# Performance work log

Hardware: AMD Instinct MI355X
Metric: run time of the kernel (lower is better)

## Reference

```python
import jax, jax.numpy as jnp
import numpy as np

D_MODEL = 768
BATCH = 4096
RANK_DIST = [(4, 512), (8, 256), (16, 128), (32, 64), (64, 32)]


@jax.custom_vjp
def jumprelu(x):
    # hard threshold at 0 in fwd; full straight-through estimator in bwd
    return x * (x > 0.0).astype(x.dtype)


def _jr_fwd(x):
    return jumprelu(x), None


def _jr_bwd(res, g):
    return (g,)


jumprelu.defvjp(_jr_fwd, _jr_bwd)


def setup_inputs() -> dict:
    key = jax.random.key(0)
    keys = jax.random.split(key, 1 + 3 * len(RANK_DIST))
    inp = {"x": jax.random.normal(keys[0], (BATCH, D_MODEL), dtype=jnp.float32)}
    for i, (n, r) in enumerate(RANK_DIST):
        kV, kU, kE = keys[1 + 3 * i], keys[2 + 3 * i], keys[3 + 3 * i]
        scale = (1.0 / (D_MODEL * r)) ** 0.25
        inp[f"V{i}"] = scale * jax.random.normal(kV, (n, r, D_MODEL), dtype=jnp.float32)
        inp[f"U{i}"] = scale * jax.random.normal(kU, (n, D_MODEL, r), dtype=jnp.float32)
        enc = jax.random.normal(kE, (n, D_MODEL), dtype=jnp.float32)
        inp[f"enc{i}"] = enc / jnp.linalg.norm(enc, axis=1, keepdims=True)
        inp[f"b{i}"] = jnp.full((n,), -1.0, dtype=jnp.float32)
    return inp


def _group_forward(x, V, U, enc, b):
    n, r, d = V.shape
    pre = x @ enc.T - b                      # (b, n)
    gate = jumprelu(pre)                     # (b, n)
    Vx = jnp.einsum("nrd,bd->nbr", V, x)    # (n, b, r)
    # fused: UVx gated by gate then summed over transforms n
    out = jnp.einsum("ndr,nbr,bn->bd", U, Vx, gate)  # (b, d)
    u_norms = jnp.linalg.norm(U.reshape(n, -1), axis=1)
    v_norms = jnp.linalg.norm(V.reshape(n, -1), axis=1)
    frob = u_norms * v_norms / jnp.sqrt(jnp.asarray(d * r, dtype=x.dtype))
    return out, gate, frob


def reference(x, V0, U0, enc0, b0, V1, U1, enc1, b1, V2, U2, enc2, b2,
              V3, U3, enc3, b3, V4, U4, enc4, b4):
    Vs = [V0, V1, V2, V3, V4]
    Us = [U0, U1, U2, U3, U4]
    encs = [enc0, enc1, enc2, enc3, enc4]
    bs = [b0, b1, b2, b3, b4]
    output = jnp.zeros_like(x)
    total_sparsity = jnp.asarray(0.0, dtype=x.dtype)
    total_active = jnp.asarray(0.0, dtype=x.dtype)
    gate_acts = []
    for V, U, enc, b in zip(Vs, Us, encs, bs):
        g_out, gate, frob = _group_forward(x, V, U, enc, b)
        output = output + g_out
        mean_abs_gate = jnp.abs(gate).mean(axis=0)
        total_sparsity = total_sparsity + (jnp.tanh(mean_abs_gate) * frob).sum()
        total_active = total_active + (gate > 0).astype(x.dtype).sum(axis=1).mean()
        gate_acts.append(gate)
    return (output, total_sparsity, total_active, *gate_acts)
```

## Files before the change

### kernel.cpp

```cpp
#include <hip/hip_runtime.h>

#define BATCH 4096
#define DM 768
#define LTOT 10240
#define NG 124

typedef __bf16 bf16x8 __attribute__((ext_vector_type(8)));
typedef short short8 __attribute__((ext_vector_type(8)));
typedef float f32x4 __attribute__((ext_vector_type(4)));
typedef float f32x16 __attribute__((ext_vector_type(16)));

struct Ptr5 { const float* p[5]; };

__device__ __forceinline__ unsigned short f2bf(float f) {
    unsigned u = __builtin_bit_cast(unsigned, f);
    unsigned r = (u + 0x7FFFu + ((u >> 16) & 1u)) >> 16;
    return (unsigned short)r;
}

__device__ __forceinline__ short8 pack8(float4 a, float4 b) {
    union { unsigned short u[8]; short8 s; } o;
    o.u[0] = f2bf(a.x); o.u[1] = f2bf(a.y); o.u[2] = f2bf(a.z); o.u[3] = f2bf(a.w);
    o.u[4] = f2bf(b.x); o.u[5] = f2bf(b.y); o.u[6] = f2bf(b.z); o.u[7] = f2bf(b.w);
    return o.s;
}


__global__ __launch_bounds__(256) void prep_k(const float* __restrict__ x,
                                              Ptr5 vp, Ptr5 up, Ptr5 ep, Ptr5 bp,
                                              unsigned short* __restrict__ vb,
                                              unsigned short* __restrict__ w2t,
                                              unsigned short* __restrict__ xb,
                                              float* __restrict__ gate_ws,
                                              float* __restrict__ outg,
                                              float* __restrict__ vslot,
                                              float* __restrict__ uslot,
                                              float* __restrict__ gslot,
                                              float* __restrict__ aslot) {
    const int basen[5] = {0, 4, 12, 28, 60};
    int bx = blockIdx.x;
    int tid = threadIdx.x;
    if (bx < 32) {
        __shared__ unsigned short lA[128 * 64];
        __shared__ unsigned short lB[128 * 64];
        __shared__ float sgs[128];
        __shared__ float sac;
        int wave = tid >> 6, lane = tid & 63;
        int wm = wave >> 1, wn = wave & 1;
        int lan15 = lane & 15, quad = lane >> 4;
        int sw = lan15 & 7;
        int m0 = bx * 128;
        f32x4 acc[4][4] = {};
        for (int k0 = 0; k0 < DM; k0 += 64) {
            __syncthreads();
            #pragma unroll
            for (int i = 0; i < 4; i++) {
                int gidx = i * 256 + tid;
                int row = gidx >> 3, kb = gidx & 7;
                int r7 = row & 7;
                int la = (row >> 3) * 512 + r7 * 64 + (kb ^ r7) * 8;
                int sidx = (m0 + row) * 192 + (k0 >> 2) + kb * 2;
                float4 a0 = ((const float4*)x)[sidx];
                float4 a1 = ((const float4*)x)[sidx + 1];
                *(short8*)(lA + la) = pack8(a0, a1);
                float4 b0 = {0.f, 0.f, 0.f, 0.f}, b1 = {0.f, 0.f, 0.f, 0.f};
                if (row < NG) {
                    int g = (row < 4) ? 0 : (row < 12) ? 1 : (row < 28) ? 2 :
                            (row < 60) ? 3 : 4;
                    int ni = row - basen[g];
                    int eidx = ni * 192 + (k0 >> 2) + kb * 2;
                    b0 = ((const float4*)ep.p[g])[eidx];
                    b1 = ((const float4*)ep.p[g])[eidx + 1];
                }
                *(short8*)(lB + la) = pack8(b0, b1);
            }
            __syncthreads();
            #pragma unroll
            for (int kk = 0; kk < 2; kk++) {
                int kb = kk * 4 + quad;
                int kel = (kb ^ sw) * 8;
                bf16x8 af[4], bfr[4];
                #pragma unroll
                for (int t = 0; t < 4; t++) {
                    short8 ra = *(const short8*)(lA + (wm * 64 + t * 16 + lan15) * 64 + kel);
                    short8 rb = *(const short8*)(lB + (wn * 64 + t * 16 + lan15) * 64 + kel);
                    af[t]  = __builtin_bit_cast(bf16x8, ra);
                    bfr[t] = __builtin_bit_cast(bf16x8, rb);
                }
                #pragma unroll
                for (int mt = 0; mt < 4; mt++)
                    #pragma unroll
                    for (int nt = 0; nt < 4; nt++)
                        acc[mt][nt] = __builtin_amdgcn_mfma_f32_16x16x32_bf16(
                            af[mt], bfr[nt], acc[mt][nt], 0, 0, 0);
            }
        }
        if (tid < 128) sgs[tid] = 0.f;
        if (tid == 0) sac = 0.f;
        __syncthreads();
        const size_t baseg[5] = {3145730ull, 3145730ull + 16384, 3145730ull + 49152,
                                 3145730ull + 114688, 3145730ull + 245760};
        float cnt = 0.f;
        #pragma unroll
        for (int nt = 0; nt < 4; nt++) {
            int col = wn * 64 + nt * 16 + lan15;
            float cs = 0.f;
            if (col < NG) {
                int g = (col < 4) ? 0 : (col < 12) ? 1 : (col < 28) ? 2 :
                        (col < 60) ? 3 : 4;
                int ni = col - basen[g];
                int w = 4 << g;
                float bv = bp.p[g][ni];
                #pragma unroll
                for (int mt = 0; mt < 4; mt++) {
                    int r0 = m0 + wm * 64 + mt * 16 + quad * 4;
                    #pragma unroll
                    for (int rg = 0; rg < 4; rg++) {
                        float pre = acc[mt][nt][rg] - bv;
                        float gt = pre > 0.f ? pre : 0.f;
                        gate_ws[(size_t)(r0 + rg) * NG + col] = gt;
                        outg[baseg[g] + (size_t)(r0 + rg) * w + ni] = gt;
                        cs += gt;
                        if (pre > 0.f) cnt += 1.f;
                    }
                }
                cs += __shfl_xor(cs, 16);
                cs += __shfl_xor(cs, 32);
                if (quad == 0) atomicAdd(&sgs[col], cs);
            }
        }
        #pragma unroll
        for (int off = 32; off > 0; off >>= 1) cnt += __shfl_xor(cnt, off);
        if (lane == 0) atomicAdd(&sac, cnt);
        __syncthreads();
        if (tid < NG) gslot[bx * NG + tid] = sgs[tid];
        if (tid == 0) aslot[bx] = sac;
    } else if (bx < 1952) {
        __shared__ float swave[4];
        int cb = bx - 32;
        int isV = cb < 960;
        int wb = isV ? cb : cb - 960;
        int g = wb / 192;
        int within = wb - g * 192;
        const float* src = isV ? vp.p[g] : up.p[g];
        int r = 512 >> g, lr = 9 - g;
        float ss = 0.f;
        #pragma unroll
        for (int i = 0; i < 8; i++) {
            int j = within * 2048 + i * 256 + tid;
            float4 v = ((const float4*)src)[j];
            ss += v.x*v.x + v.y*v.y + v.z*v.z + v.w*v.w;
            ushort4 o;
            o.x = f2bf(v.x); o.y = f2bf(v.y); o.z = f2bf(v.z); o.w = f2bf(v.w);
            if (isV) {
                ((ushort4*)vb)[(size_t)(g * 192 + within) * 2048 + i * 256 + tid] = o;
            } else {
                int idx = j * 4;
                int rr = idx & (r - 1);
                int t2 = idx >> lr;
                int d  = t2 % DM;
                int n  = t2 / DM;
                size_t dst = (size_t)d * LTOT + (size_t)(g << 11) + (size_t)n * r + rr;
                *(ushort4*)(w2t + dst) = o;
            }
        }
        #pragma unroll
        for (int off = 32; off > 0; off >>= 1) ss += __shfl_down(ss, off);
        if ((tid & 63) == 0) swave[tid >> 6] = ss;
        __syncthreads();
        if (tid == 0) {
            float t = (swave[0] + swave[1]) + (swave[2] + swave[3]);
            (isV ? vslot : uslot)[wb] = t;
        }
    } else {
        int base = (bx - 1952) * 2048;
        #pragma unroll
        for (int i = 0; i < 8; i++) {
            int j = base + i * 256 + tid;
            float4 v = ((const float4*)x)[j];
            ushort4 o;
            o.x = f2bf(v.x); o.y = f2bf(v.y); o.z = f2bf(v.z); o.w = f2bf(v.w);
            ((ushort4*)xb)[j] = o;
        }
    }
}

template <int ROWS, int NT>
__device__ __forceinline__ void stage(const unsigned short* __restrict__ src, int ld,
                                      unsigned short* lds, int wv, int lane) {
    int rsub = lane >> 3;
    int colb = ((lane ^ rsub) & 7) * 8;
    #pragma unroll
    for (int i = 0; i < ROWS * 8 / NT; i++) {
        int c = i * (NT / 64) + wv;
        const unsigned short* gp = src + (size_t)(c * 8 + rsub) * ld + colb;
        __builtin_amdgcn_global_load_lds((const __attribute__((address_space(1))) void*)gp,
                                         (__attribute__((address_space(3))) void*)(lds + c * 512),
                                         16, 0, 0);
    }
}

template <int BM, int BN, int NT>
__global__ __launch_bounds__(NT) void gemm_nt(const unsigned short* __restrict__ A,
                                              const unsigned short* __restrict__ Bm,
                                              int Kblk, int lda, int ldb,
                                              void* __restrict__ Cout,
                                              const float* __restrict__ gate, int ldc) {
    __shared__ unsigned short lA[BM * 64];
    __shared__ unsigned short lB[BN * 64];
    int tid = threadIdx.x, wave = tid >> 6, lane = tid & 63;
    constexpr int WN = BN / 64;
    int wm = wave / WN, wn = wave % WN;
    int m0 = blockIdx.x * BM, n0 = blockIdx.y * BN;
    A  += (size_t)m0 * lda;
    Bm += (size_t)n0 * ldb;
    f32x4 acc[4][4] = {};
    int lan15 = lane & 15, quad = lane >> 4;
    int sw = lan15 & 7;

    for (int k0 = 0; k0 < Kblk; k0 += 64) {
        stage<BM, NT>(A + k0, lda, lA, wave, lane);
        stage<BN, NT>(Bm + k0, ldb, lB, wave, lane);
        __syncthreads();
        #pragma unroll
        for (int kk = 0; kk < 2; kk++) {
            int kb = kk * 4 + quad;
            int kel = (kb ^ sw) * 8;
            bf16x8 af[4], bfr[4];
            #pragma unroll
            for (int t = 0; t < 4; t++) {
                short8 ra = *(const short8*)(lA + (size_t)(wm * 64 + t * 16 + lan15) * 64 + kel);
                short8 rb = *(const short8*)(lB + (size_t)(wn * 64 + t * 16 + lan15) * 64 + kel);
                af[t]  = __builtin_bit_cast(bf16x8, ra);
                bfr[t] = __builtin_bit_cast(bf16x8, rb);
            }
            #pragma unroll
            for (int mt = 0; mt < 4; mt++)
                #pragma unroll
                for (int nt = 0; nt < 4; nt++)
                    acc[mt][nt] = __builtin_amdgcn_mfma_f32_16x16x32_bf16(af[mt], bfr[nt],
                                                                          acc[mt][nt], 0, 0, 0);
        }
        __syncthreads();
    }

    const int basen[5] = {0, 4, 12, 28, 60};
    unsigned short* H = (unsigned short*)Cout;
    #pragma unroll
    for (int mt = 0; mt < 4; mt++) {
        __syncthreads();
        #pragma unroll
        for (int nt = 0; nt < 4; nt++) {
            int col = n0 + wn * 64 + nt * 16 + lan15;
            int g = col >> 11;
            int ngl = basen[g] + ((col & 2047) >> (9 - g));
            #pragma unroll
            for (int rg = 0; rg < 4; rg++) {
                int grow = m0 + wm * 64 + mt * 16 + quad * 4 + rg;
                float gv = gate[(size_t)grow * NG + ngl];
                lA[wave * 1024 + (quad * 4 + rg) * 64 + nt * 16 + lan15] =
                    f2bf(acc[mt][nt][rg] * gv);
            }
        }
        __syncthreads();
        #pragma unroll
        for (int i = 0; i < 2; i++) {
            int f = i * NT + tid;
            int R = f >> 5;
            int u = f & 31;
            int wv2 = ((R >> 4) << 2) + (u >> 3);
            short8 vread = *(const short8*)(lA + wv2 * 1024 + (R & 15) * 64 + (u & 7) * 8);
            int grow = m0 + (R >> 4) * 64 + mt * 16 + (R & 15);
            *(short8*)(H + (size_t)grow * ldc + n0 + u * 8) = vread;
        }
    }
}

__global__ __launch_bounds__(256) void gemm32_nt(const unsigned short* __restrict__ A,
                                                 const unsigned short* __restrict__ Bm,
                                                 int Kblk, int lda, int ldb,
                                                 float* __restrict__ P, int ldc) {
    __shared__ unsigned short lA[128 * 64];
    __shared__ unsigned short lB[128 * 64];
    int tid = threadIdx.x, wave = tid >> 6, lane = tid & 63;
    int wm = wave >> 1, wn = wave & 1;
    int m0 = blockIdx.x * 128, n0 = blockIdx.y * 128;
    A  += (size_t)m0 * lda + (size_t)blockIdx.z * Kblk;
    Bm += (size_t)n0 * ldb + (size_t)blockIdx.z * Kblk;
    f32x16 acc[2][2] = {};
    int lan31 = lane & 31, half = lane >> 5;
    int sw = lan31 & 7;

    for (int k0 = 0; k0 < Kblk; k0 += 64) {
        stage<128, 256>(A + k0, lda, lA, wave, lane);
        stage<128, 256>(Bm + k0, ldb, lB, wave, lane);
        __syncthreads();
        #pragma unroll
        for (int kk = 0; kk < 4; kk++) {
            int kb = kk * 2 + half;
            int kel = (kb ^ sw) * 8;
            bf16x8 af[2], bfr[2];
            #pragma unroll
            for (int t = 0; t < 2; t++) {
                short8 ra = *(const short8*)(lA + (size_t)(wm * 64 + t * 32 + lan31) * 64 + kel);
                short8 rb = *(const short8*)(lB + (size_t)(wn * 64 + t * 32 + lan31) * 64 + kel);
                af[t]  = __builtin_bit_cast(bf16x8, ra);
                bfr[t] = __builtin_bit_cast(bf16x8, rb);
            }
            #pragma unroll
            for (int mt = 0; mt < 2; mt++)
                #pragma unroll
                for (int nt = 0; nt < 2; nt++)
                    acc[mt][nt] = __builtin_amdgcn_mfma_f32_32x32x16_bf16(af[mt], bfr[nt],
                                                                          acc[mt][nt], 0, 0, 0);
        }
        __syncthreads();
    }

    P += (size_t)blockIdx.z * gridDim.x * 128 * ldc;
    #pragma unroll
    for (int nt = 0; nt < 2; nt++) {
        int col = n0 + wn * 64 + nt * 32 + lan31;
        #pragma unroll
        for (int mt = 0; mt < 2; mt++) {
            int rbase = m0 + wm * 64 + mt * 32 + 4 * half;
            #pragma unroll
            for (int reg = 0; reg < 16; reg++) {
                int row = rbase + (reg & 3) + 8 * (reg >> 2);
                P[(size_t)row * ldc + col] = acc[mt][nt][reg];
            }
        }
    }
}


__global__ __launch_bounds__(256) void reduce_k(const float4* __restrict__ P,
                                                float4* __restrict__ out, int quarter,
                                                const float* __restrict__ vslot,
                                                const float* __restrict__ uslot,
                                                const float* __restrict__ gslot,
                                                const float* __restrict__ aslot,
                                                float* __restrict__ o2) {
    int i = blockIdx.x * 256 + threadIdx.x;
    float4 a = P[i], b = P[i + quarter], c = P[i + 2 * quarter], d = P[i + 3 * quarter];
    float4 o;
    o.x = (a.x + b.x) + (c.x + d.x);
    o.y = (a.y + b.y) + (c.y + d.y);
    o.z = (a.z + b.z) + (c.z + d.z);
    o.w = (a.w + b.w) + (c.w + d.w);
    out[i] = o;
    if (blockIdx.x == 0) {
        __shared__ float sh[128];
        const int basen[5] = {0, 4, 12, 28, 60};
        int t = threadIdx.x;
        if (t < 128) {
            float v = 0.f;
            if (t < NG) {
                int g = (t < 4) ? 0 : (t < 12) ? 1 : (t < 28) ? 2 : (t < 60) ? 3 : 4;
                int nloc = t - basen[g];
                int bpseg = 48 >> g;
                float vs = 0.f, us = 0.f;
                int base = g * 192 + nloc * bpseg;
                for (int j = 0; j < bpseg; j++) { vs += vslot[base + j]; us += uslot[base + j]; }
                float gs = 0.f;
                for (int bb = 0; bb < 32; bb++) gs += gslot[bb * NG + t];
                float rr = (float)(512 >> g);
                float mean = gs * (1.0f / BATCH);
                float frob = sqrtf(us * vs) / sqrtf(768.0f * rr);
                v = tanhf(mean) * frob;
            }
            sh[t] = v;
        }
        if (t == 128) {
            float asum = 0.f;
            for (int bb = 0; bb < 32; bb++) asum += aslot[bb];
            o2[1] = asum * (1.0f / BATCH);
        }
        __syncthreads();
        for (int s = 64; s > 0; s >>= 1) {
            if (threadIdx.x < s) sh[threadIdx.x] += sh[threadIdx.x + s];
            __syncthreads();
        }
        if (threadIdx.x == 0) o2[0] = sh[0];
    }
}


extern "C" void kernel_launch(void* const* d_in, const int* in_sizes, int n_in,
                              void* d_out, int out_size, void* d_ws, size_t ws_size,
                              hipStream_t stream) {
    const float* x = (const float*)d_in[0];
    Ptr5 vp, up, ep, bp;
    for (int g = 0; g < 5; g++) {
        vp.p[g] = (const float*)d_in[1 + 4 * g];
        up.p[g] = (const float*)d_in[2 + 4 * g];
        ep.p[g] = (const float*)d_in[3 + 4 * g];
        bp.p[g] = (const float*)d_in[4 + 4 * g];
    }
    float* out = (float*)d_out;
    char* ws = (char*)d_ws;
    size_t off = 0;
    unsigned short* xb   = (unsigned short*)(ws + off); off += (size_t)BATCH * DM * 2;
    unsigned short* vb   = (unsigned short*)(ws + off); off += (size_t)LTOT * DM * 2;
    unsigned short* w2t  = (unsigned short*)(ws + off); off += (size_t)LTOT * DM * 2;
    float* gate_ws       = (float*)(ws + off);          off += (size_t)BATCH * NG * 4;
    float* vslot         = (float*)(ws + off);          off += 960 * 4;
    float* uslot         = (float*)(ws + off);          off += 960 * 4;
    float* gslot         = (float*)(ws + off);          off += 32 * NG * 4;
    float* aslot         = (float*)(ws + off);          off += 32 * 4 + 256;
    size_t fixed = off;
    int CB = BATCH;
    while (CB > 128 && fixed + (size_t)CB * LTOT * 2 + 4ull * CB * DM * 4 > ws_size) CB >>= 1;
    unsigned short* Hg  = (unsigned short*)(ws + fixed);
    float* partial      = (float*)(ws + fixed + (size_t)CB * LTOT * 2);

    prep_k<<<dim3(2336), 256, 0, stream>>>(
        x, vp, up, ep, bp, vb, w2t, xb, gate_ws, out,
        vslot, uslot, gslot, aslot);

    int nch = BATCH / CB;
    for (int c = 0; c < nch; c++) {
        gemm_nt<128, 256, 512><<<dim3(CB / 128, LTOT / 256, 1), 512, 0, stream>>>(
            xb + (size_t)c * CB * DM, vb, DM, DM, DM,
            (void*)Hg, gate_ws + (size_t)c * CB * NG, LTOT);
        gemm32_nt<<<dim3(CB / 128, DM / 128, 4), 256, 0, stream>>>(
            Hg, w2t, LTOT / 4, LTOT, LTOT, partial, DM);
        reduce_k<<<dim3(CB * 192 / 256), 256, 0, stream>>>(
            (const float4*)partial, (float4*)(out + (size_t)c * CB * DM), CB * DM / 4,
            vslot, uslot, gslot, aslot, out + (size_t)BATCH * DM);
    }
}
```

Baseline: 341.8 us.

## Retile second GEMM to 256x128 blocks with 16x16x32 MFMA

Replaces the 128x128-tile second GEMM (32x32x16 MFMA, 2x2 wave grid) with a 256x128 tile where each wave owns 64 rows and all 128 columns, using 16x16x32 bf16 MFMA. Each block reuses every staged B tile across twice as many rows, which cuts global and LDS traffic per FLOP. In exchange the grid has half as many blocks (a small split-K grid) and each thread holds more accumulators, so occupancy and load balance may suffer. The minimum chunk size rises to 256.

```diff
diff --git a/kernel.cpp b/kernel.cpp
--- a/kernel.cpp
+++ b/kernel.cpp
@@ -8,7 +8,6 @@
 typedef __bf16 bf16x8 __attribute__((ext_vector_type(8)));
 typedef short short8 __attribute__((ext_vector_type(8)));
 typedef float f32x4 __attribute__((ext_vector_type(4)));
-typedef float f32x16 __attribute__((ext_vector_type(16)));
 
 struct Ptr5 { const float* p[5]; };
 
@@ -276,59 +275,63 @@
     }
 }
 
-__global__ __launch_bounds__(256) void gemm32_nt(const unsigned short* __restrict__ A,
-                                                 const unsigned short* __restrict__ Bm,
-                                                 int Kblk, int lda, int ldb,
-                                                 float* __restrict__ P, int ldc) {
-    __shared__ unsigned short lA[128 * 64];
+__global__ __launch_bounds__(256) void gemm2_nt(const unsigned short* __restrict__ A,
+                                                const unsigned short* __restrict__ Bm,
+                                                int Kblk, int lda, int ldb,
+                                                float* __restrict__ P, int ldc) {
+    __shared__ unsigned short lA[256 * 64];
     __shared__ unsigned short lB[128 * 64];
     int tid = threadIdx.x, wave = tid >> 6, lane = tid & 63;
-    int wm = wave >> 1, wn = wave & 1;
-    int m0 = blockIdx.x * 128, n0 = blockIdx.y * 128;
+    int m0 = blockIdx.x * 256, n0 = blockIdx.y * 128;
     A  += (size_t)m0 * lda + (size_t)blockIdx.z * Kblk;
     Bm += (size_t)n0 * ldb + (size_t)blockIdx.z * Kblk;
-    f32x16 acc[2][2] = {};
-    int lan31 = lane & 31, half = lane >> 5;
-    int sw = lan31 & 7;
+    f32x4 acc[4][8] = {};
+    int lan15 = lane & 15, quad = lane >> 4;
+    int sw = lan15 & 7;
 
     for (int k0 = 0; k0 < Kblk; k0 += 64) {
-        stage<128, 256>(A + k0, lda, lA, wave, lane);
+        stage<256, 256>(A + k0, lda, lA, wave, lane);
         stage<128, 256>(Bm + k0, ldb, lB, wave, lane);
         __syncthreads();
         #pragma unroll
-        for (int kk = 0; kk < 4; kk++) {
-            int kb = kk * 2 + half;
+        for (int kk = 0; kk < 2; kk++) {
+            int kb = kk * 4 + quad;
             int kel = (kb ^ sw) * 8;
-            bf16x8 af[2], bfr[2];
-            #pragma unroll
-            for (int t = 0; t < 2; t++) {
-                short8 ra = *(const short8*)(lA + (size_t)(wm * 64 + t * 32 + lan31) * 64 + kel);
-                short8 rb = *(const short8*)(lB + (size_t)(wn * 64 + t * 32 + lan31) * 64 + kel);
-                af[t]  = __builtin_bit_cast(bf16x8, ra);
-                bfr[t] = __builtin_bit_cast(bf16x8, rb);
-            }
-            #pragma unroll
-            for (int mt = 0; mt < 2; mt++)
-                #pragma unroll
-                for (int nt = 0; nt < 2; nt++)
-                    acc[mt][nt] = __builtin_amdgcn_mfma_f32_32x32x16_bf16(af[mt], bfr[nt],
-                                                                          acc[mt][nt], 0, 0, 0);
-        }
-        __syncthreads();
-    }
-
-    P += (size_t)blockIdx.z * gridDim.x * 128 * ldc;
+            bf16x8 af[4];
+            #pragma unroll
+            for (int t = 0; t < 4; t++) {
+                short8 ra = *(const short8*)(lA + (size_t)(wave * 64 + t * 16 + lan15) * 64 + kel);
+                af[t] = __builtin_bit_cast(bf16x8, ra);
+            }
+            #pragma unroll
+            for (int nh = 0; nh < 2; nh++) {
+                bf16x8 bfr[4];
+                #pragma unroll
+                for (int t = 0; t < 4; t++) {
+                    short8 rb = *(const short8*)(lB + (size_t)((nh * 4 + t) * 16 + lan15) * 64 + kel);
+                    bfr[t] = __builtin_bit_cast(bf16x8, rb);
+                }
+                #pragma unroll
+                for (int mt = 0; mt < 4; mt++)
+                    #pragma unroll
+                    for (int nt = 0; nt < 4; nt++)
+                        acc[mt][nh * 4 + nt] = __builtin_amdgcn_mfma_f32_16x16x32_bf16(
+                            af[mt], bfr[nt], acc[mt][nh * 4 + nt], 0, 0, 0);
+            }
+        }
+        __syncthreads();
+    }
+
+    P += (size_t)blockIdx.z * (size_t)gridDim.x * 256 * ldc;
     #pragma unroll
-    for (int nt = 0; nt < 2; nt++) {
-        int col = n0 + wn * 64 + nt * 32 + lan31;
-        #pragma unroll
-        for (int mt = 0; mt < 2; mt++) {
-            int rbase = m0 + wm * 64 + mt * 32 + 4 * half;
-            #pragma unroll
-            for (int reg = 0; reg < 16; reg++) {
-                int row = rbase + (reg & 3) + 8 * (reg >> 2);
-                P[(size_t)row * ldc + col] = acc[mt][nt][reg];
-            }
+    for (int mt = 0; mt < 4; mt++) {
+        #pragma unroll
+        for (int rg = 0; rg < 4; rg++) {
+            int row = m0 + wave * 64 + mt * 16 + quad * 4 + rg;
+            float* pr = P + (size_t)row * ldc + n0 + lan15;
+            #pragma unroll
+            for (int nt = 0; nt < 8; nt++)
+                pr[nt * 16] = acc[mt][nt][rg];
         }
     }
 }
@@ -410,7 +413,7 @@
     float* aslot         = (float*)(ws + off);          off += 32 * 4 + 256;
     size_t fixed = off;
     int CB = BATCH;
-    while (CB > 128 && fixed + (size_t)CB * LTOT * 2 + 4ull * CB * DM * 4 > ws_size) CB >>= 1;
+    while (CB > 256 && fixed + (size_t)CB * LTOT * 2 + 4ull * CB * DM * 4 > ws_size) CB >>= 1;
     unsigned short* Hg  = (unsigned short*)(ws + fixed);
     float* partial      = (float*)(ws + fixed + (size_t)CB * LTOT * 2);
 
@@ -423,7 +426,7 @@
         gemm_nt<128, 256, 512><<<dim3(CB / 128, LTOT / 256, 1), 512, 0, stream>>>(
             xb + (size_t)c * CB * DM, vb, DM, DM, DM,
             (void*)Hg, gate_ws + (size_t)c * CB * NG, LTOT);
-        gemm32_nt<<<dim3(CB / 128, DM / 128, 4), 256, 0, stream>>>(
+        gemm2_nt<<<dim3(CB / 256, DM / 128, 4), 256, 0, stream>>>(
             Hg, w2t, LTOT / 4, LTOT, LTOT, partial, DM);
         reduce_k<<<dim3(CB * 192 / 256), 256, 0, stream>>>(
             (const float4*)partial, (float4*)(out + (size_t)c * CB * DM), CB * DM / 4,
```

New measurement: 412.9 us. 20.8% more time.
